# Performance work log

Measured on AMD Instinct MI355X. Metric: run time of the kernel, lower is better.

The kernel has to match this reference:

```python
import jax, jax.numpy as jnp
import numpy as np

B, S, E = 2, 2048, 1024
NH, NKV = 16, 4
HD = E // NH
GS = NH // NKV


def setup_inputs() -> dict:
    key = jax.random.key(0)
    ks = jax.random.split(key, 8)
    sc = 0.02
    query = jax.random.normal(ks[0], (B, S, E), dtype=jnp.float32)
    key_t = jax.random.normal(ks[1], (B, S, E), dtype=jnp.float32)
    value = jax.random.normal(ks[2], (B, S, E), dtype=jnp.float32)
    # causal mask, broadcast shape [1,1,S,S] as in source (unsqueeze(0).unsqueeze(0))
    attn_mask = jnp.tril(jnp.ones((S, S), dtype=bool))[None, None]
    Wq = jax.random.normal(ks[3], (NH * HD, E), dtype=jnp.float32) * sc
    Wk = jax.random.normal(ks[4], (NKV * HD, E), dtype=jnp.float32) * sc
    Wv = jax.random.normal(ks[5], (NKV * HD, E), dtype=jnp.float32) * sc
    Wo = jax.random.normal(ks[6], (E, NH * HD), dtype=jnp.float32) * sc
    return {"query": query, "key": key_t, "value": value, "attn_mask": attn_mask,
            "Wq": Wq, "Wk": Wk, "Wv": Wv, "Wo": Wo}


def reference(query, key, value, attn_mask, Wq, Wk, Wv, Wo):
    # projections (nn.Linear, bias=False: y = x @ W.T)
    q = (query @ Wq.T).reshape(B, S, NH, HD).transpose(0, 2, 1, 3)   # [B,NH,S,HD]
    k = (key @ Wk.T).reshape(B, S, NKV, HD).transpose(0, 2, 1, 3)    # [B,NKV,S,HD]
    v = (value @ Wv.T).reshape(B, S, NKV, HD).transpose(0, 2, 1, 3)  # [B,NKV,S,HD]
    # repeat_interleave over head dim to match query heads
    k = jnp.repeat(k, GS, axis=1)  # [B,NH,S,HD]
    v = jnp.repeat(v, GS, axis=1)
    scale = 1.0 / np.sqrt(HD).astype(np.float32)
    scores = jnp.einsum('bhqd,bhkd->bhqk', q, k) * scale  # [B,NH,S,S]
    scores = jnp.where(attn_mask, scores, -jnp.inf)
    weights = jax.nn.softmax(scores, axis=-1)
    out = jnp.einsum('bhqk,bhkd->bhqd', weights, v)        # [B,NH,S,HD]
    out = out.transpose(0, 2, 1, 3).reshape(B, S, NH * HD)
    return out @ Wo.T  # [B,S,E]
```

## Files before the change

kernel.cpp:

```cpp
#include <hip/hip_runtime.h>
#include <hip/hip_bf16.h>

typedef __attribute__((ext_vector_type(8))) short bf16x8;
typedef __attribute__((ext_vector_type(4))) float f32x4;

#define MFMA16(a, b, c) __builtin_amdgcn_mfma_f32_16x16x32_bf16((a), (b), (c), 0, 0, 0)
#define ASYNC16(g, l)                                                     \
    __builtin_amdgcn_global_load_lds(                                     \
        (const __attribute__((address_space(1))) void*)(g),               \
        (__attribute__((address_space(3))) void*)(l), 16, 0, 0)

constexpr int B_ = 2, S_ = 2048, E_ = 1024, NH_ = 16, NKV_ = 4, HD_ = 64;

__global__ __launch_bounds__(256) void cvt_all(
    const float* __restrict__ s0, const float* __restrict__ s1,
    const float* __restrict__ s2, const float* __restrict__ s3,
    const float* __restrict__ s4, const float* __restrict__ s5,
    const float* __restrict__ s6,
    __hip_bfloat16* __restrict__ d0, __hip_bfloat16* __restrict__ d1,
    __hip_bfloat16* __restrict__ d2, __hip_bfloat16* __restrict__ d3,
    __hip_bfloat16* __restrict__ d4, __hip_bfloat16* __restrict__ d5,
    __hip_bfloat16* __restrict__ d6)
{
    int id = blockIdx.x;
    const float* s;
    __hip_bfloat16* d;
    if (id < 6144) {
        const int which = id >> 11;
        s = which == 0 ? s0 : (which == 1 ? s1 : s2);
        d = which == 0 ? d0 : (which == 1 ? d1 : d2);
        id &= 2047;
    } else if (id < 6656) { s = s3; d = d3; id -= 6144; }
    else if (id < 7168)   { s = s4; d = d4; id -= 6656; }
    else if (id < 7296)   { s = s5; d = d5; id -= 7168; }
    else                  { s = s6; d = d6; id -= 7296; }

    const size_t i = ((size_t)id * 256 + threadIdx.x) * 8;
    const float4 f0 = *reinterpret_cast<const float4*>(s + i);
    const float4 f1 = *reinterpret_cast<const float4*>(s + i + 4);
    union { __hip_bfloat16 h[8]; uint4 u; } t;
    t.h[0] = __float2bfloat16(f0.x); t.h[1] = __float2bfloat16(f0.y);
    t.h[2] = __float2bfloat16(f0.z); t.h[3] = __float2bfloat16(f0.w);
    t.h[4] = __float2bfloat16(f1.x); t.h[5] = __float2bfloat16(f1.y);
    t.h[6] = __float2bfloat16(f1.z); t.h[7] = __float2bfloat16(f1.w);
    *reinterpret_cast<uint4*>(d + i) = t.u;
}

__device__ __forceinline__ void gemm_core(
    const __hip_bfloat16* __restrict__ A,
    const __hip_bfloat16* __restrict__ W,
    void* __restrict__ C,
    const int N, const int mode, const int m0, const int n0,
    __hip_bfloat16* sA, __hip_bfloat16* sW)
{
    const int tid  = threadIdx.x;
    const int l    = tid & 63;
    const int w    = tid >> 6;
    const int quad = l >> 4;
    const int lan  = l & 15;
    const int wm   = (w >> 1) * 32;
    const int wn   = (w & 1) * 64;

    const int srow  = w * 8 + (l >> 3);
    const int scolL = (l & 7) * 8;
    const int scolG = ((l & 7) ^ (l >> 3)) * 8;

    f32x4 acc[2][4] = {};

#define STAGE(buf, kb)                                                    \
    {                                                                     \
        _Pragma("unroll")                                                 \
        for (int q = 0; q < 2; ++q) {                                     \
            const int r_ = q * 32 + srow;                                 \
            ASYNC16(A + (size_t)(m0 + r_) * E_ + (kb) + scolG,            \
                    sA + (buf) * 4096 + r_ * 64 + scolL);                 \
        }                                                                 \
        _Pragma("unroll")                                                 \
        for (int q = 0; q < 4; ++q) {                                     \
            const int r_ = q * 32 + srow;                                 \
            ASYNC16(W + (size_t)(n0 + r_) * E_ + (kb) + scolG,            \
                    sW + (buf) * 8192 + r_ * 64 + scolL);                 \
        }                                                                 \
    }

    STAGE(0, 0)
    int cur = 0;
#pragma unroll 1
    for (int t = 0; t < 16; ++t) {
        __syncthreads();
        if (t < 15) STAGE(cur ^ 1, (t + 1) * 64)

#pragma unroll
        for (int kk = 0; kk < 2; ++kk) {
            bf16x8 af[2], bf[4];
            const int ca = ((kk * 4 + quad) ^ (lan & 7)) * 8;
#pragma unroll
            for (int i = 0; i < 2; ++i)
                af[i] = *reinterpret_cast<const bf16x8*>(
                    sA + cur * 4096 + (wm + i * 16 + lan) * 64 + ca);
#pragma unroll
            for (int j = 0; j < 4; ++j)
                bf[j] = *reinterpret_cast<const bf16x8*>(
                    sW + cur * 8192 + (wn + j * 16 + lan) * 64 + ca);
#pragma unroll
            for (int i = 0; i < 2; ++i)
#pragma unroll
                for (int j = 0; j < 4; ++j)
                    acc[i][j] = MFMA16(af[i], bf[j], acc[i][j]);
        }
        cur ^= 1;
    }
#undef STAGE

#pragma unroll
    for (int i = 0; i < 2; ++i)
#pragma unroll
        for (int j = 0; j < 4; ++j)
#pragma unroll
            for (int r = 0; r < 4; ++r) {
                const int gm = m0 + wm + i * 16 + quad * 4 + r;
                const int gn = n0 + wn + j * 16 + lan;
                const float v = acc[i][j][r];
                if (mode == 2) {
                    ((float*)C)[(size_t)gm * N + gn] = v;
                } else {
                    const __hip_bfloat16 hv = __float2bfloat16(v);
                    if (mode == 0)
                        ((__hip_bfloat16*)C)[(size_t)gm * N + gn] = hv;
                    else
                        ((__hip_bfloat16*)C)
                            [((size_t)(gm >> 11) * N + gn) * (size_t)S_ +
                             (gm & 2047)] = hv;
                }
            }
}

__global__ __launch_bounds__(256) void gemm_qkv(
    const __hip_bfloat16* __restrict__ qb, const __hip_bfloat16* __restrict__ kb,
    const __hip_bfloat16* __restrict__ vb, const __hip_bfloat16* __restrict__ Wqb,
    const __hip_bfloat16* __restrict__ Wkb, const __hip_bfloat16* __restrict__ Wvb,
    __hip_bfloat16* __restrict__ QO, __hip_bfloat16* __restrict__ Kws,
    __hip_bfloat16* __restrict__ VT)
{
    __shared__ __hip_bfloat16 sA[2 * 4096];
    __shared__ __hip_bfloat16 sW[2 * 8192];
    int id = blockIdx.x;
    const __hip_bfloat16 *A, *W;
    void* C;
    int N, mode, bx, by;
    if (id < 512)      { A = qb; W = Wqb; C = QO;  N = 1024; mode = 0; bx = id & 7; by = id >> 3; }
    else if (id < 640) { id -= 512; A = kb; W = Wkb; C = Kws; N = 256; mode = 0; bx = id & 1; by = id >> 1; }
    else               { id -= 640; A = vb; W = Wvb; C = VT;  N = 256; mode = 1; bx = id & 1; by = id >> 1; }
    gemm_core(A, W, C, N, mode, by * 64, bx * 128, sA, sW);
}

__global__ __launch_bounds__(256) void gemm_out(
    const __hip_bfloat16* __restrict__ QO, const __hip_bfloat16* __restrict__ Wob,
    float* __restrict__ out)
{
    __shared__ __hip_bfloat16 sA[2 * 4096];
    __shared__ __hip_bfloat16 sW[2 * 8192];
    const int id = blockIdx.x;
    gemm_core(QO, Wob, out, 1024, 2, (id >> 3) * 64, (id & 7) * 128, sA, sW);
}

__global__ __launch_bounds__(256) void attn(
    __hip_bfloat16* QO,
    const __hip_bfloat16* __restrict__ Kp,
    const __hip_bfloat16* __restrict__ VT)
{
    __shared__ __hip_bfloat16 sK[64][64];
    __shared__ __hip_bfloat16 sV[64][64];

    const int bx   = blockIdx.x;
    const int h    = blockIdx.y;
    const int b    = blockIdx.z;
    const int hk   = h >> 2;
    const int tid  = threadIdx.x;
    const int l    = tid & 63;
    const int w    = tid >> 6;
    const int quad = l >> 4;
    const int lan  = l & 15;
    const bool hi  = quad >= 2;
    const float KSC = 0.125f * 1.44269504088896340736f;

    const int idxA = (((quad & 1) * 32) + lan) * 4;
    const int idxB = idxA + 64;

    const int kr  = tid >> 2;
    const int s0c = (tid & 3) * 2;
    const int sw0 = (s0c ^ (kr & 7)) * 8;
    const int sw1 = ((s0c + 1) ^ (kr & 7)) * 8;
    const int kc  = s0c * 8;

    const int swq0 = (quad ^ (lan & 7)) * 8;
    const int swq1 = ((4 + quad) ^ (lan & 7)) * 8;

    const __hip_bfloat16* kg =
        Kp + ((size_t)((b * S_ + kr) * NKV_) + hk) * HD_ + kc;
    const __hip_bfloat16* vg =
        VT + ((size_t)((b * NKV_ + hk) * HD_) + kr) * S_ + kc;
    const size_t kstride = (size_t)64 * NKV_ * HD_;

    for (int half = 0; half < 2; ++half) {
        const int qt  = half ? (31 - bx) : bx;
        const int qr0 = qt * 64 + w * 16;
        const int qme = qr0 + lan;

        const __hip_bfloat16* qp =
            QO + ((size_t)((b * S_ + qme) * NH_) + h) * HD_ + quad * 8;
        const bf16x8 aq0 = *reinterpret_cast<const bf16x8*>(qp);
        const bf16x8 aq1 = *reinterpret_cast<const bf16x8*>(qp + 32);

        float m_i = -3.0e38f, l_i = 0.f;
        f32x4 acc_o[4] = {};

        uint4 kv0 = *reinterpret_cast<const uint4*>(kg);
        uint4 kv1 = *reinterpret_cast<const uint4*>(kg + 8);
        uint4 vv0 = *reinterpret_cast<const uint4*>(vg);
        uint4 vv1 = *reinterpret_cast<const uint4*>(vg + 8);

        for (int kt = 0; kt <= qt; ++kt) {
            __syncthreads();
            *reinterpret_cast<uint4*>(&sK[kr][sw0]) = kv0;
            *reinterpret_cast<uint4*>(&sK[kr][sw1]) = kv1;
            *reinterpret_cast<uint4*>(&sV[kr][sw0]) = vv0;
            *reinterpret_cast<uint4*>(&sV[kr][sw1]) = vv1;
            __syncthreads();

            if (kt < qt) {
                const __hip_bfloat16* kn = kg + (size_t)(kt + 1) * kstride;
                const __hip_bfloat16* vn = vg + (size_t)(kt + 1) * 64;
                kv0 = *reinterpret_cast<const uint4*>(kn);
                kv1 = *reinterpret_cast<const uint4*>(kn + 8);
                vv0 = *reinterpret_cast<const uint4*>(vn);
                vv1 = *reinterpret_cast<const uint4*>(vn + 8);
            }

            f32x4 accs[4] = {};
#pragma unroll
            for (int j = 0; j < 4; ++j) {
                bf16x8 bk0 = *reinterpret_cast<const bf16x8*>(&sK[j * 16 + lan][swq0]);
                accs[j] = MFMA16(bk0, aq0, accs[j]);
                bf16x8 bk1 = *reinterpret_cast<const bf16x8*>(&sK[j * 16 + lan][swq1]);
                accs[j] = MFMA16(bk1, aq1, accs[j]);
            }

            if (kt == qt) {
#pragma unroll
                for (int j = 0; j < 4; ++j)
#pragma unroll
                    for (int r = 0; r < 4; ++r) {
                        const int kcg = kt * 64 + j * 16 + quad * 4 + r;
                        if (kcg > qme) accs[j][r] = -1e30f;
                    }
            }

            float tm = accs[0][0];
#pragma unroll
            for (int j = 0; j < 4; ++j)
#pragma unroll
                for (int r = 0; r < 4; ++r) tm = fmaxf(tm, accs[j][r]);
            tm = fmaxf(tm, __shfl_xor(tm, 16));
            tm = fmaxf(tm, __shfl_xor(tm, 32));

            if (__any((tm - m_i) * KSC > 8.0f)) {
                const float mnew  = fmaxf(m_i, tm);
                const float alpha = exp2f((m_i - mnew) * KSC);
                l_i *= alpha;
                m_i  = mnew;
#pragma unroll
                for (int dd = 0; dd < 4; ++dd)
#pragma unroll
                    for (int r = 0; r < 4; ++r) acc_o[dd][r] *= alpha;
            }

            float ps = 0.f;
#pragma unroll
            for (int j = 0; j < 4; ++j)
#pragma unroll
                for (int r = 0; r < 4; ++r) {
                    const float p = exp2f((accs[j][r] - m_i) * KSC);
                    accs[j][r] = p;
                    ps += p;
                }
            ps += __shfl_xor(ps, 16);
            ps += __shfl_xor(ps, 32);
            l_i += ps;

            uint pk[4][2];
#pragma unroll
            for (int j = 0; j < 4; ++j)
#pragma unroll
                for (int hh = 0; hh < 2; ++hh) {
                    union { __hip_bfloat16 bh[2]; uint u; } t;
                    t.bh[0] = __float2bfloat16(accs[j][2 * hh]);
                    t.bh[1] = __float2bfloat16(accs[j][2 * hh + 1]);
                    pk[j][hh] = t.u;
                }

#pragma unroll
            for (int kk = 0; kk < 2; ++kk) {
                union { uint u[4]; bf16x8 v; } pb;
#pragma unroll
                for (int w2 = 0; w2 < 4; ++w2) {
                    const int idx = (w2 & 2) ? idxB : idxA;
                    const uint a = (uint)__builtin_amdgcn_ds_bpermute(
                        idx, (int)pk[2 * kk][w2 & 1]);
                    const uint bb = (uint)__builtin_amdgcn_ds_bpermute(
                        idx, (int)pk[2 * kk + 1][w2 & 1]);
                    pb.u[w2] = hi ? bb : a;
                }
#pragma unroll
                for (int dd = 0; dd < 4; ++dd) {
                    const int swv = ((kk * 4 + quad) ^ (lan & 7)) * 8;
                    bf16x8 av = *reinterpret_cast<const bf16x8*>(
                        &sV[dd * 16 + lan][swv]);
                    acc_o[dd] = MFMA16(av, pb.v, acc_o[dd]);
                }
            }
        }

        const float inv = 1.0f / l_i;
        __hip_bfloat16* op =
            QO + ((size_t)((b * S_ + qme) * NH_) + h) * HD_ + quad * 4;
#pragma unroll
        for (int dd = 0; dd < 4; ++dd) {
            union { __hip_bfloat16 bh[4]; uint2 u; } t;
#pragma unroll
            for (int r = 0; r < 4; ++r)
                t.bh[r] = __float2bfloat16(acc_o[dd][r] * inv);
            *reinterpret_cast<uint2*>(op + dd * 16) = t.u;
        }
    }
}

extern "C" void kernel_launch(void* const* d_in, const int* in_sizes, int n_in,
                              void* d_out, int out_size, void* d_ws, size_t ws_size,
                              hipStream_t stream) {
    const float* q  = (const float*)d_in[0];
    const float* k  = (const float*)d_in[1];
    const float* v  = (const float*)d_in[2];
    const float* Wq = (const float*)d_in[4];
    const float* Wk = (const float*)d_in[5];
    const float* Wv = (const float*)d_in[6];
    const float* Wo = (const float*)d_in[7];

    __hip_bfloat16* ws = (__hip_bfloat16*)d_ws;
    __hip_bfloat16* qb   = ws;
    __hip_bfloat16* kb   = qb  + 4194304;
    __hip_bfloat16* vb   = kb  + 4194304;
    __hip_bfloat16* QO   = vb  + 4194304;
    __hip_bfloat16* Kws  = QO  + 4194304;
    __hip_bfloat16* VT   = Kws + 1048576;
    __hip_bfloat16* Wqb  = VT  + 1048576;
    __hip_bfloat16* Wob  = Wqb + 1048576;
    __hip_bfloat16* Wkb  = Wob + 1048576;
    __hip_bfloat16* Wvb  = Wkb + 262144;

    cvt_all<<<dim3(7424), 256, 0, stream>>>(
        q, k, v, Wq, Wo, Wk, Wv, qb, kb, vb, Wqb, Wob, Wkb, Wvb);

    gemm_qkv<<<dim3(768), 256, 0, stream>>>(
        qb, kb, vb, Wqb, Wkb, Wvb, QO, Kws, VT);

    attn<<<dim3(16, NH_, B_), 256, 0, stream>>>(QO, Kws, VT);

    gemm_out<<<dim3(512), 256, 0, stream>>>(QO, Wob, (float*)d_out);
}
```

Measured before the change: 210.7 us.

## Rewrite attention with 32x32 MFMA tiles, LDS P staging, one query tile per block

The attention kernel moves from 16x16x32 MFMAs to 32x32x16 MFMAs, so each wave handles 32 query rows and 64 keys with fewer LDS reads per FLOP. Each block now runs 2 waves on a single query tile, with tiles launched heaviest-first, instead of 4 waves processing a paired light/heavy tile. P is passed to the PV MFMA through a per-wave LDS buffer rather than ds_bpermute shuffles. The trade-offs are higher register pressure from the f32x16 accumulators, more blocks with less intra-block load balancing, and extra LDS traffic for P.

Result: slower. 311.3 us (+47.8%).

```diff
diff --git a/kernel.cpp b/kernel.cpp
--- a/kernel.cpp
+++ b/kernel.cpp
@@ -3,8 +3,10 @@
 
 typedef __attribute__((ext_vector_type(8))) short bf16x8;
 typedef __attribute__((ext_vector_type(4))) float f32x4;
+typedef __attribute__((ext_vector_type(16))) float f32x16;
 
 #define MFMA16(a, b, c) __builtin_amdgcn_mfma_f32_16x16x32_bf16((a), (b), (c), 0, 0, 0)
+#define MFMA32(a, b, c) __builtin_amdgcn_mfma_f32_32x32x16_bf16((a), (b), (c), 0, 0, 0)
 #define ASYNC16(g, l)                                                     \
     __builtin_amdgcn_global_load_lds(                                     \
         (const __attribute__((address_space(1))) void*)(g),               \
@@ -164,37 +166,32 @@
     gemm_core(QO, Wob, out, 1024, 2, (id >> 3) * 64, (id & 7) * 128, sA, sW);
 }
 
-__global__ __launch_bounds__(256) void attn(
+__global__ __launch_bounds__(128) void attn(
     __hip_bfloat16* QO,
     const __hip_bfloat16* __restrict__ Kp,
     const __hip_bfloat16* __restrict__ VT)
 {
     __shared__ __hip_bfloat16 sK[64][64];
     __shared__ __hip_bfloat16 sV[64][64];
-
-    const int bx   = blockIdx.x;
-    const int h    = blockIdx.y;
-    const int b    = blockIdx.z;
-    const int hk   = h >> 2;
-    const int tid  = threadIdx.x;
-    const int l    = tid & 63;
-    const int w    = tid >> 6;
-    const int quad = l >> 4;
-    const int lan  = l & 15;
-    const bool hi  = quad >= 2;
+    __shared__ __hip_bfloat16 sP[2][32][72];
+
+    const int qt  = 31 - blockIdx.x;
+    const int h   = blockIdx.y;
+    const int b   = blockIdx.z;
+    const int hk  = h >> 2;
+    const int tid = threadIdx.x;
+    const int l   = tid & 63;
+    const int w   = tid >> 6;
+    const int q32 = l & 31;
+    const int h5  = l >> 5;
     const float KSC = 0.125f * 1.44269504088896340736f;
 
-    const int idxA = (((quad & 1) * 32) + lan) * 4;
-    const int idxB = idxA + 64;
-
-    const int kr  = tid >> 2;
-    const int s0c = (tid & 3) * 2;
-    const int sw0 = (s0c ^ (kr & 7)) * 8;
-    const int sw1 = ((s0c + 1) ^ (kr & 7)) * 8;
-    const int kc  = s0c * 8;
-
-    const int swq0 = (quad ^ (lan & 7)) * 8;
-    const int swq1 = ((4 + quad) ^ (lan & 7)) * 8;
+    const int kr = tid >> 1;
+    const int sb = (tid & 1) * 4;
+    const int kc = (tid & 1) * 32;
+    int swz[4];
+#pragma unroll
+    for (int j = 0; j < 4; ++j) swz[j] = ((sb + j) ^ (kr & 7)) * 8;
 
     const __hip_bfloat16* kg =
         Kp + ((size_t)((b * S_ + kr) * NKV_) + hk) * HD_ + kc;
@@ -202,136 +199,143 @@
         VT + ((size_t)((b * NKV_ + hk) * HD_) + kr) * S_ + kc;
     const size_t kstride = (size_t)64 * NKV_ * HD_;
 
-    for (int half = 0; half < 2; ++half) {
-        const int qt  = half ? (31 - bx) : bx;
-        const int qr0 = qt * 64 + w * 16;
-        const int qme = qr0 + lan;
-
-        const __hip_bfloat16* qp =
-            QO + ((size_t)((b * S_ + qme) * NH_) + h) * HD_ + quad * 8;
-        const bf16x8 aq0 = *reinterpret_cast<const bf16x8*>(qp);
-        const bf16x8 aq1 = *reinterpret_cast<const bf16x8*>(qp + 32);
-
-        float m_i = -3.0e38f, l_i = 0.f;
-        f32x4 acc_o[4] = {};
-
-        uint4 kv0 = *reinterpret_cast<const uint4*>(kg);
-        uint4 kv1 = *reinterpret_cast<const uint4*>(kg + 8);
-        uint4 vv0 = *reinterpret_cast<const uint4*>(vg);
-        uint4 vv1 = *reinterpret_cast<const uint4*>(vg + 8);
-
-        for (int kt = 0; kt <= qt; ++kt) {
-            __syncthreads();
-            *reinterpret_cast<uint4*>(&sK[kr][sw0]) = kv0;
-            *reinterpret_cast<uint4*>(&sK[kr][sw1]) = kv1;
-            *reinterpret_cast<uint4*>(&sV[kr][sw0]) = vv0;
-            *reinterpret_cast<uint4*>(&sV[kr][sw1]) = vv1;
-            __syncthreads();
-
-            if (kt < qt) {
-                const __hip_bfloat16* kn = kg + (size_t)(kt + 1) * kstride;
-                const __hip_bfloat16* vn = vg + (size_t)(kt + 1) * 64;
-                kv0 = *reinterpret_cast<const uint4*>(kn);
-                kv1 = *reinterpret_cast<const uint4*>(kn + 8);
-                vv0 = *reinterpret_cast<const uint4*>(vn);
-                vv1 = *reinterpret_cast<const uint4*>(vn + 8);
-            }
-
-            f32x4 accs[4] = {};
+    const int qr0 = qt * 64 + w * 32;
+    const int qme = qr0 + q32;
+
+    const __hip_bfloat16* qp =
+        QO + ((size_t)((b * S_ + qme) * NH_) + h) * HD_ + h5 * 8;
+    bf16x8 aq[4];
+#pragma unroll
+    for (int dg = 0; dg < 4; ++dg)
+        aq[dg] = *reinterpret_cast<const bf16x8*>(qp + dg * 16);
+
+    float m_i = -3.0e38f, l_i = 0.f;
+    f32x16 acc_o0 = {}, acc_o1 = {};
+
+    uint4 kv[4], vv[4];
+#pragma unroll
+    for (int j = 0; j < 4; ++j) {
+        kv[j] = *reinterpret_cast<const uint4*>(kg + j * 8);
+        vv[j] = *reinterpret_cast<const uint4*>(vg + j * 8);
+    }
+
+    for (int kt = 0; kt <= qt; ++kt) {
+        __syncthreads();
+#pragma unroll
+        for (int j = 0; j < 4; ++j) {
+            *reinterpret_cast<uint4*>(&sK[kr][swz[j]]) = kv[j];
+            *reinterpret_cast<uint4*>(&sV[kr][swz[j]]) = vv[j];
+        }
+        __syncthreads();
+
+        if (kt < qt) {
+            const __hip_bfloat16* kn = kg + (size_t)(kt + 1) * kstride;
+            const __hip_bfloat16* vn = vg + (size_t)(kt + 1) * 64;
 #pragma unroll
             for (int j = 0; j < 4; ++j) {
-                bf16x8 bk0 = *reinterpret_cast<const bf16x8*>(&sK[j * 16 + lan][swq0]);
-                accs[j] = MFMA16(bk0, aq0, accs[j]);
-                bf16x8 bk1 = *reinterpret_cast<const bf16x8*>(&sK[j * 16 + lan][swq1]);
-                accs[j] = MFMA16(bk1, aq1, accs[j]);
-            }
-
-            if (kt == qt) {
-#pragma unroll
-                for (int j = 0; j < 4; ++j)
-#pragma unroll
-                    for (int r = 0; r < 4; ++r) {
-                        const int kcg = kt * 64 + j * 16 + quad * 4 + r;
-                        if (kcg > qme) accs[j][r] = -1e30f;
-                    }
-            }
-
-            float tm = accs[0][0];
-#pragma unroll
-            for (int j = 0; j < 4; ++j)
-#pragma unroll
-                for (int r = 0; r < 4; ++r) tm = fmaxf(tm, accs[j][r]);
-            tm = fmaxf(tm, __shfl_xor(tm, 16));
-            tm = fmaxf(tm, __shfl_xor(tm, 32));
-
-            if (__any((tm - m_i) * KSC > 8.0f)) {
-                const float mnew  = fmaxf(m_i, tm);
-                const float alpha = exp2f((m_i - mnew) * KSC);
-                l_i *= alpha;
-                m_i  = mnew;
-#pragma unroll
-                for (int dd = 0; dd < 4; ++dd)
-#pragma unroll
-                    for (int r = 0; r < 4; ++r) acc_o[dd][r] *= alpha;
-            }
-
-            float ps = 0.f;
-#pragma unroll
-            for (int j = 0; j < 4; ++j)
-#pragma unroll
-                for (int r = 0; r < 4; ++r) {
-                    const float p = exp2f((accs[j][r] - m_i) * KSC);
-                    accs[j][r] = p;
-                    ps += p;
-                }
-            ps += __shfl_xor(ps, 16);
-            ps += __shfl_xor(ps, 32);
-            l_i += ps;
-
-            uint pk[4][2];
-#pragma unroll
-            for (int j = 0; j < 4; ++j)
-#pragma unroll
-                for (int hh = 0; hh < 2; ++hh) {
-                    union { __hip_bfloat16 bh[2]; uint u; } t;
-                    t.bh[0] = __float2bfloat16(accs[j][2 * hh]);
-                    t.bh[1] = __float2bfloat16(accs[j][2 * hh + 1]);
-                    pk[j][hh] = t.u;
-                }
-
-#pragma unroll
-            for (int kk = 0; kk < 2; ++kk) {
-                union { uint u[4]; bf16x8 v; } pb;
-#pragma unroll
-                for (int w2 = 0; w2 < 4; ++w2) {
-                    const int idx = (w2 & 2) ? idxB : idxA;
-                    const uint a = (uint)__builtin_amdgcn_ds_bpermute(
-                        idx, (int)pk[2 * kk][w2 & 1]);
-                    const uint bb = (uint)__builtin_amdgcn_ds_bpermute(
-                        idx, (int)pk[2 * kk + 1][w2 & 1]);
-                    pb.u[w2] = hi ? bb : a;
-                }
-#pragma unroll
-                for (int dd = 0; dd < 4; ++dd) {
-                    const int swv = ((kk * 4 + quad) ^ (lan & 7)) * 8;
-                    bf16x8 av = *reinterpret_cast<const bf16x8*>(
-                        &sV[dd * 16 + lan][swv]);
-                    acc_o[dd] = MFMA16(av, pb.v, acc_o[dd]);
-                }
-            }
-        }
-
-        const float inv = 1.0f / l_i;
-        __hip_bfloat16* op =
-            QO + ((size_t)((b * S_ + qme) * NH_) + h) * HD_ + quad * 4;
-#pragma unroll
-        for (int dd = 0; dd < 4; ++dd) {
-            union { __hip_bfloat16 bh[4]; uint2 u; } t;
-#pragma unroll
-            for (int r = 0; r < 4; ++r)
-                t.bh[r] = __float2bfloat16(acc_o[dd][r] * inv);
-            *reinterpret_cast<uint2*>(op + dd * 16) = t.u;
-        }
+                kv[j] = *reinterpret_cast<const uint4*>(kn + j * 8);
+                vv[j] = *reinterpret_cast<const uint4*>(vn + j * 8);
+            }
+        }
+
+        f32x16 accs0 = {}, accs1 = {};
+#pragma unroll
+        for (int dg = 0; dg < 4; ++dg) {
+            const int r0 = q32;
+            const int c0 = ((dg * 2 + h5) ^ (r0 & 7)) * 8;
+            bf16x8 ak0 = *reinterpret_cast<const bf16x8*>(&sK[r0][c0]);
+            accs0 = MFMA32(ak0, aq[dg], accs0);
+            const int r1 = 32 + q32;
+            const int c1 = ((dg * 2 + h5) ^ (r1 & 7)) * 8;
+            bf16x8 ak1 = *reinterpret_cast<const bf16x8*>(&sK[r1][c1]);
+            accs1 = MFMA32(ak1, aq[dg], accs1);
+        }
+
+        if (kt == qt) {
+#pragma unroll
+            for (int r = 0; r < 16; ++r) {
+                const int kb0 = kt * 64 + (r & 3) + 8 * (r >> 2) + 4 * h5;
+                if (kb0 > qme)      accs0[r] = -1e30f;
+                if (kb0 + 32 > qme) accs1[r] = -1e30f;
+            }
+        }
+
+        float tm = -3.0e38f;
+#pragma unroll
+        for (int r = 0; r < 16; ++r) {
+            tm = fmaxf(tm, accs0[r]);
+            tm = fmaxf(tm, accs1[r]);
+        }
+        tm = fmaxf(tm, __shfl_xor(tm, 32));
+
+        if (__any((tm - m_i) * KSC > 8.0f)) {
+            const float mnew  = fmaxf(m_i, tm);
+            const float alpha = exp2f((m_i - mnew) * KSC);
+            l_i *= alpha;
+            m_i  = mnew;
+#pragma unroll
+            for (int r = 0; r < 16; ++r) {
+                acc_o0[r] *= alpha;
+                acc_o1[r] *= alpha;
+            }
+        }
+
+        float ps = 0.f;
+#pragma unroll
+        for (int r = 0; r < 16; ++r) {
+            const float p0 = exp2f((accs0[r] - m_i) * KSC);
+            const float p1 = exp2f((accs1[r] - m_i) * KSC);
+            accs0[r] = p0; accs1[r] = p1;
+            ps += p0 + p1;
+        }
+        ps += __shfl_xor(ps, 32);
+        l_i += ps;
+
+#pragma unroll
+        for (int q4 = 0; q4 < 4; ++q4) {
+            union { __hip_bfloat16 bh[4]; uint2 u; } t0, t1;
+#pragma unroll
+            for (int i = 0; i < 4; ++i) {
+                t0.bh[i] = __float2bfloat16(accs0[q4 * 4 + i]);
+                t1.bh[i] = __float2bfloat16(accs1[q4 * 4 + i]);
+            }
+            const int kb0 = 8 * q4 + 4 * h5;
+            *reinterpret_cast<uint2*>(&sP[w][q32][kb0])      = t0.u;
+            *reinterpret_cast<uint2*>(&sP[w][q32][32 + kb0]) = t1.u;
+        }
+
+        bf16x8 pb[4];
+#pragma unroll
+        for (int kg16 = 0; kg16 < 4; ++kg16)
+            pb[kg16] = *reinterpret_cast<const bf16x8*>(
+                &sP[w][q32][kg16 * 16 + h5 * 8]);
+#pragma unroll
+        for (int kg16 = 0; kg16 < 4; ++kg16) {
+            const int r0 = q32;
+            const int c0 = ((kg16 * 2 + h5) ^ (r0 & 7)) * 8;
+            bf16x8 av0 = *reinterpret_cast<const bf16x8*>(&sV[r0][c0]);
+            acc_o0 = MFMA32(av0, pb[kg16], acc_o0);
+            const int r1 = 32 + q32;
+            const int c1 = ((kg16 * 2 + h5) ^ (r1 & 7)) * 8;
+            bf16x8 av1 = *reinterpret_cast<const bf16x8*>(&sV[r1][c1]);
+            acc_o1 = MFMA32(av1, pb[kg16], acc_o1);
+        }
+    }
+
+    const float inv = 1.0f / l_i;
+    __hip_bfloat16* op =
+        QO + ((size_t)((b * S_ + qme) * NH_) + h) * HD_;
+#pragma unroll
+    for (int q4 = 0; q4 < 4; ++q4) {
+        union { __hip_bfloat16 bh[4]; uint2 u; } t0, t1;
+#pragma unroll
+        for (int i = 0; i < 4; ++i) {
+            t0.bh[i] = __float2bfloat16(acc_o0[q4 * 4 + i] * inv);
+            t1.bh[i] = __float2bfloat16(acc_o1[q4 * 4 + i] * inv);
+        }
+        const int d0 = 8 * q4 + 4 * h5;
+        *reinterpret_cast<uint2*>(op + d0)      = t0.u;
+        *reinterpret_cast<uint2*>(op + 32 + d0) = t1.u;
     }
 }
 
@@ -364,7 +368,7 @@
     gemm_qkv<<<dim3(768), 256, 0, stream>>>(
         qb, kb, vb, Wqb, Wkb, Wvb, QO, Kws, VT);
 
-    attn<<<dim3(16, NH_, B_), 256, 0, stream>>>(QO, Kws, VT);
+    attn<<<dim3(32, NH_, B_), 128, 0, stream>>>(QO, Kws, VT);
 
     gemm_out<<<dim3(512), 256, 0, stream>>>(QO, Wob, (float*)d_out);
 }
```
